# Optimization experiments

Hardware: AMD Instinct MI355X
Metric: run time of the kernel (lower is better)

## Reference

```python
import jax, jax.numpy as jnp
import numpy as np

N_NODES = 100000
N_EDGES = 1600000
IN_FEATS = 128
H_FEATS = 64
N_CONVS = 3
POLY_ORDER = 4
NUM_CLASSES = 2


def setup_inputs() -> dict:
    key = jax.random.key(0)
    ks = jax.random.split(key, 12)
    def w(k, shape):
        fan_in = shape[0]
        return jax.random.normal(k, shape, dtype=jnp.float32) / jnp.sqrt(jnp.float32(fan_in))
    return {
        "feature": jax.random.normal(ks[0], (N_NODES, IN_FEATS), dtype=jnp.float32),
        "src": jax.random.randint(ks[1], (N_EDGES,), 0, N_NODES, dtype=jnp.int32),
        "dst": jax.random.randint(ks[2], (N_EDGES,), 0, N_NODES, dtype=jnp.int32),
        "W1": w(ks[3], (IN_FEATS, H_FEATS)),
        "b1": jnp.zeros((H_FEATS,), dtype=jnp.float32),
        "W2": w(ks[4], (H_FEATS, H_FEATS)),
        "b2": jnp.zeros((H_FEATS,), dtype=jnp.float32),
        "thetas": jax.random.normal(ks[5], (N_CONVS, POLY_ORDER), dtype=jnp.float32) * 0.5,
        "Wm1": w(ks[6], (N_CONVS * H_FEATS, H_FEATS)),
        "bm1": jnp.zeros((H_FEATS,), dtype=jnp.float32),
        "Wm2": w(ks[7], (H_FEATS, NUM_CLASSES)),
        "bm2": jnp.zeros((NUM_CLASSES,), dtype=jnp.float32),
    }


def _poly_conv(theta, feat, src, dst, d_invsqrt, n_nodes):
    # h = sum_k theta[k] * L^k feat, L = I - D^-1/2 A D^-1/2 (applied iteratively)
    out = theta[0] * feat
    for k in range(1, theta.shape[0]):
        m = feat * d_invsqrt                      # [N, H]
        agg = jax.ops.segment_sum(m[src], dst, num_segments=n_nodes)  # copy_u -> sum
        feat = feat - agg * d_invsqrt
        out = out + theta[k] * feat
    return out


def reference(feature, src, dst, W1, b1, W2, b2, thetas, Wm1, bm1, Wm2, bm2):
    n_nodes = feature.shape[0]
    # in-degrees, clamp(min=1), D^-1/2
    deg = jax.ops.segment_sum(jnp.ones_like(dst, dtype=jnp.float32), dst, num_segments=n_nodes)
    d_invsqrt = jnp.power(jnp.clip(deg, 1.0, None), -0.5)[:, None]   # [N, 1]
    # ChiGNN trunk: linear -> ReLU -> linear2 -> ReLU
    h = jax.nn.relu(feature @ W1 + b1)
    h = jax.nn.relu(h @ W2 + b2)
    # N_CONVS polynomial convolutions, concatenated on feature axis
    h_final = jnp.concatenate(
        [_poly_conv(thetas[i], h, src, dst, d_invsqrt, n_nodes) for i in range(thetas.shape[0])],
        axis=-1,
    )  # [N, N_CONVS * H]
    # 2-layer MLP head
    out = jax.nn.relu(h_final @ Wm1 + bm1) @ Wm2 + bm2   # [N, num_classes]
    return out
```

## Files before the change

kernel.cpp:

```cpp
#include <hip/hip_runtime.h>
#include <hip/hip_fp16.h>
#include <math.h>

#define N_NODES 100000
#define N_EDGES 1600000
#define IN_FEATS 128
#define H_FEATS 64
#define NBUK 500
#define BSZ 200
#define NBA 512
#define ACHUNK 3125

typedef _Float16 f16x8 __attribute__((ext_vector_type(8)));
typedef float f32x4 __attribute__((ext_vector_type(4)));

__global__ __launch_bounds__(256) void bucketA_kernel(const int* __restrict__ dst,
                                                      int* __restrict__ blkcnt) {
    __shared__ int cnt[NBUK];
    int t = threadIdx.x;
    for (int i = t; i < NBUK; i += 256) cnt[i] = 0;
    __syncthreads();
    int e0 = blockIdx.x * ACHUNK;
    for (int e = e0 + t; e < e0 + ACHUNK; e += 256)
        atomicAdd(&cnt[dst[e] / BSZ], 1);
    __syncthreads();
    for (int i = t; i < NBUK; i += 256)
        blkcnt[blockIdx.x * NBUK + i] = cnt[i];
}

__global__ __launch_bounds__(512) void bucketB1_kernel(const int* __restrict__ blkcnt,
                                                       int* __restrict__ boff,
                                                       int* __restrict__ buktot) {
    __shared__ int tmp[512];
    int b = blockIdx.x;
    int t = threadIdx.x;
    int v = blkcnt[t * NBUK + b];
    tmp[t] = v;
    __syncthreads();
    #pragma unroll
    for (int off = 1; off < 512; off <<= 1) {
        int x = (t >= off) ? tmp[t - off] : 0;
        __syncthreads();
        tmp[t] += x;
        __syncthreads();
    }
    boff[t * NBUK + b] = tmp[t] - v;
    if (t == 511) buktot[b] = tmp[511];
}

__global__ __launch_bounds__(512) void bucketB2_kernel(const int* __restrict__ buktot,
                                                       int* __restrict__ bukbase,
                                                       int* __restrict__ rowp) {
    __shared__ int tmp[512];
    int t = threadIdx.x;
    int v = (t < NBUK) ? buktot[t] : 0;
    tmp[t] = v;
    __syncthreads();
    #pragma unroll
    for (int off = 1; off < 512; off <<= 1) {
        int x = (t >= off) ? tmp[t - off] : 0;
        __syncthreads();
        tmp[t] += x;
        __syncthreads();
    }
    if (t < NBUK) bukbase[t] = tmp[t] - v;
    if (t == 0) rowp[N_NODES] = N_EDGES;
}

__global__ __launch_bounds__(256) void bucketC_kernel(const int* __restrict__ src,
                                                      const int* __restrict__ dst,
                                                      const int* __restrict__ boff,
                                                      const int* __restrict__ bukbase,
                                                      int* __restrict__ ebuck) {
    __shared__ int sbase[NBUK];
    __shared__ int cur[NBUK];
    int t = threadIdx.x;
    for (int i = t; i < NBUK; i += 256) {
        sbase[i] = bukbase[i] + boff[blockIdx.x * NBUK + i];
        cur[i] = 0;
    }
    __syncthreads();
    int e0 = blockIdx.x * ACHUNK;
    for (int e = e0 + t; e < e0 + ACHUNK; e += 256) {
        int d = dst[e];
        int b = d / BSZ;
        int r = atomicAdd(&cur[b], 1);
        ebuck[sbase[b] + r] = (src[e] << 8) | (d - b * BSZ);
    }
}

__global__ __launch_bounds__(256) void bucketD1_kernel(const int* __restrict__ ebuck,
                                                       const int* __restrict__ bukbase,
                                                       const int* __restrict__ buktot,
                                                       int* __restrict__ rowp,
                                                       float* __restrict__ dinv) {
    __shared__ int deg[BSZ];
    __shared__ int tmp[256];
    int t = threadIdx.x;
    int buk = blockIdx.x;
    int nlo = buk * BSZ;
    int base = bukbase[buk];
    int cnt = buktot[buk];
    for (int i = t; i < BSZ; i += 256) deg[i] = 0;
    __syncthreads();
    for (int k = t; k < cnt; k += 256)
        atomicAdd(&deg[ebuck[base + k] & 255], 1);
    __syncthreads();
    int v = (t < BSZ) ? deg[t] : 0;
    tmp[t] = v;
    __syncthreads();
    #pragma unroll
    for (int off = 1; off < 256; off <<= 1) {
        int x = (t >= off) ? tmp[t - off] : 0;
        __syncthreads();
        tmp[t] += x;
        __syncthreads();
    }
    if (t < BSZ) {
        rowp[nlo + t] = base + tmp[t] - v;
        dinv[nlo + t] = rsqrtf(fmaxf((float)v, 1.0f));
    }
}

__global__ __launch_bounds__(256) void bucketD2_kernel(const int* __restrict__ ebuck,
                                                       const int* __restrict__ bukbase,
                                                       const int* __restrict__ buktot,
                                                       const int* __restrict__ rowp,
                                                       const float* __restrict__ dinv,
                                                       int2* __restrict__ epack) {
    __shared__ int rp[BSZ];
    __shared__ int cur2[BSZ];
    int t = threadIdx.x;
    int buk = blockIdx.x;
    int nlo = buk * BSZ;
    int base = bukbase[buk];
    int cnt = buktot[buk];
    for (int i = t; i < BSZ; i += 256) { rp[i] = rowp[nlo + i]; cur2[i] = 0; }
    __syncthreads();
    for (int k = t; k < cnt; k += 256) {
        int p = ebuck[base + k];
        int ld = p & 255;
        int s = p >> 8;
        int r = atomicAdd(&cur2[ld], 1);
        epack[rp[ld] + r] = make_int2(s, __float_as_int(dinv[s]));
    }
}

__global__ __launch_bounds__(256) void prep_kernel(const float* __restrict__ thetas,
                                                   const float* __restrict__ Wm1,
                                                   const float* __restrict__ W1,
                                                   const float* __restrict__ W2,
                                                   __half* __restrict__ Bpack,
                                                   __half* __restrict__ W1p,
                                                   __half* __restrict__ W2p) {
    int u = blockIdx.x * 256 + threadIdx.x;
    if (u < 16384) {
        int j = u & 7, lane = (u >> 3) & 63, frag = u >> 9;
        int nt = frag & 3, s = frag >> 2;
        int k = 32 * s + ((lane >> 4) << 3) + j;
        int q = k >> 6, f = k & 63;
        int n = nt * 16 + (lane & 15);
        float acc = 0.f;
        #pragma unroll
        for (int c = 0; c < 3; ++c)
            acc = fmaf(thetas[c * 4 + q], Wm1[(c * 64 + f) * 64 + n], acc);
        Bpack[u] = __float2half(acc);
    } else if (u < 16384 + 8192) {
        int v = u - 16384;
        int j = v & 7, lane = (v >> 3) & 63, frag = v >> 9;
        int nt = frag & 3, s = frag >> 2;
        int k = 32 * s + ((lane >> 4) << 3) + j;
        int n = nt * 16 + (lane & 15);
        W1p[v] = __float2half(W1[k * 64 + n]);
    } else if (u < 16384 + 8192 + 4096) {
        int v = u - 24576;
        int j = v & 7, lane = (v >> 3) & 63, frag = v >> 9;
        int nt = frag & 3, s2 = frag >> 2;
        int k = 32 * s2 + ((lane >> 4) << 3) + j;
        int n = nt * 16 + (lane & 15);
        W2p[v] = __float2half(W2[k * 64 + n]);
    }
}

__global__ __launch_bounds__(256) void trunk_mfma_kernel(
    const float* __restrict__ X, const __half* __restrict__ W1p, const float* __restrict__ b1,
    const __half* __restrict__ W2p, const float* __restrict__ b2, __half* __restrict__ H)
{
    __shared__ __half hl[4][1024];
    int t = threadIdx.x;
    int wv = t >> 6, lane = t & 63;
    int r_lo = lane & 15;
    int g = lane >> 4;
    char* myl = (char*)hl[wv];

    int tile = blockIdx.x * 4 + wv;
    if (tile >= 6250) return;

    const f16x8* w1f = (const f16x8*)W1p;
    const f16x8* w2f = (const f16x8*)W2p;
    f16x8 w1b[16], w2b[8];
    #pragma unroll
    for (int f = 0; f < 16; ++f) w1b[f] = w1f[f * 64 + lane];
    #pragma unroll
    for (int f = 0; f < 8; ++f)  w2b[f] = w2f[f * 64 + lane];
    float b1v[4], b2v[4];
    #pragma unroll
    for (int nt = 0; nt < 4; ++nt) {
        b1v[nt] = b1[nt * 16 + r_lo];
        b2v[nt] = b2[nt * 16 + r_lo];
    }

    int row0 = tile * 16;
    const float* xb = X + (size_t)(row0 + r_lo) * IN_FEATS + g * 8;
    f16x8 a1[4];
    #pragma unroll
    for (int s = 0; s < 4; ++s) {
        float4 f0 = *(const float4*)(xb + 32 * s);
        float4 f1 = *(const float4*)(xb + 32 * s + 4);
        f16x8 a;
        a[0] = (_Float16)f0.x; a[1] = (_Float16)f0.y;
        a[2] = (_Float16)f0.z; a[3] = (_Float16)f0.w;
        a[4] = (_Float16)f1.x; a[5] = (_Float16)f1.y;
        a[6] = (_Float16)f1.z; a[7] = (_Float16)f1.w;
        a1[s] = a;
    }
    f32x4 acc1[4];
    #pragma unroll
    for (int nt = 0; nt < 4; ++nt) acc1[nt] = (f32x4){0.f, 0.f, 0.f, 0.f};
    #pragma unroll
    for (int s = 0; s < 4; ++s)
        #pragma unroll
        for (int nt = 0; nt < 4; ++nt)
            acc1[nt] = __builtin_amdgcn_mfma_f32_16x16x32_f16(a1[s], w1b[s * 4 + nt], acc1[nt], 0, 0, 0);
    #pragma unroll
    for (int nt = 0; nt < 4; ++nt)
        #pragma unroll
        for (int reg = 0; reg < 4; ++reg) {
            int r = g * 4 + reg;
            int c = nt * 16 + r_lo;
            int byte = (r * 128 + c * 2) ^ ((r & 7) << 4);
            *(__half*)(myl + byte) = __float2half(fmaxf(acc1[nt][reg] + b1v[nt], 0.f));
        }
    f16x8 a2[2];
    #pragma unroll
    for (int s2 = 0; s2 < 2; ++s2) {
        int byte = (r_lo * 128 + 64 * s2 + g * 16) ^ ((r_lo & 7) << 4);
        a2[s2] = *(const f16x8*)(myl + byte);
    }
    f32x4 acc2[4];
    #pragma unroll
    for (int nt = 0; nt < 4; ++nt) acc2[nt] = (f32x4){0.f, 0.f, 0.f, 0.f};
    #pragma unroll
    for (int s2 = 0; s2 < 2; ++s2)
        #pragma unroll
        for (int nt = 0; nt < 4; ++nt)
            acc2[nt] = __builtin_amdgcn_mfma_f32_16x16x32_f16(a2[s2], w2b[s2 * 4 + nt], acc2[nt], 0, 0, 0);
    #pragma unroll
    for (int nt = 0; nt < 4; ++nt)
        #pragma unroll
        for (int reg = 0; reg < 4; ++reg) {
            int r = g * 4 + reg;
            int c = nt * 16 + r_lo;
            int byte = (r * 128 + c * 2) ^ ((r & 7) << 4);
            *(__half*)(myl + byte) = __float2half(fmaxf(acc2[nt][reg] + b2v[nt], 0.f));
        }
    #pragma unroll
    for (int h2 = 0; h2 < 2; ++h2) {
        int R = (lane >> 3) + 8 * h2;
        int w = lane & 7;
        int byte = (R * 128 + 16 * (w ^ (R & 7)));
        f16x8 hv = *(const f16x8*)(myl + byte);
        *(f16x8*)(H + (size_t)(row0 + R) * 64 + w * 8) = hv;
    }
}

__global__ __launch_bounds__(256) void gather_kernel(
    const __half* __restrict__ Fprev, const int* __restrict__ rowp,
    const int2* __restrict__ epack, const float* __restrict__ dinv,
    __half* __restrict__ Fnew)
{
    int wv = __builtin_amdgcn_readfirstlane(threadIdx.x >> 6);
    int wid = blockIdx.x * 4 + wv;
    int lane = threadIdx.x & 63;
    int beg = rowp[wid], end = rowp[wid + 1];
    float acc = 0.0f;
    int j = beg;
    for (; j + 15 < end; j += 16) {
        int2 e[16];
        #pragma unroll
        for (int q = 0; q < 16; ++q) e[q] = epack[j + q];
        float v[16];
        #pragma unroll
        for (int q = 0; q < 16; ++q)
            v[q] = __half2float(Fprev[(size_t)e[q].x * 64 + lane]);
        #pragma unroll
        for (int q = 0; q < 16; ++q)
            acc = fmaf(v[q], __int_as_float(e[q].y), acc);
    }
    for (; j + 7 < end; j += 8) {
        int2 e[8];
        #pragma unroll
        for (int q = 0; q < 8; ++q) e[q] = epack[j + q];
        float v[8];
        #pragma unroll
        for (int q = 0; q < 8; ++q)
            v[q] = __half2float(Fprev[(size_t)e[q].x * 64 + lane]);
        #pragma unroll
        for (int q = 0; q < 8; ++q)
            acc = fmaf(v[q], __int_as_float(e[q].y), acc);
    }
    for (; j + 3 < end; j += 4) {
        int2 e[4];
        #pragma unroll
        for (int q = 0; q < 4; ++q) e[q] = epack[j + q];
        float v[4];
        #pragma unroll
        for (int q = 0; q < 4; ++q)
            v[q] = __half2float(Fprev[(size_t)e[q].x * 64 + lane]);
        #pragma unroll
        for (int q = 0; q < 4; ++q)
            acc = fmaf(v[q], __int_as_float(e[q].y), acc);
    }
    for (; j < end; ++j) {
        int2 e = epack[j];
        acc = fmaf(__half2float(Fprev[(size_t)e.x * 64 + lane]), __int_as_float(e.y), acc);
    }
    float self = __half2float(Fprev[(size_t)wid * 64 + lane]);
    Fnew[(size_t)wid * 64 + lane] = __float2half(self - acc * dinv[wid]);
}

__global__ __launch_bounds__(256) void final_mfma_kernel(
    const __half* __restrict__ L0h, const __half* __restrict__ Bpack,
    const float* __restrict__ Wm2, const float* __restrict__ bm1,
    const float* __restrict__ bm2, float* __restrict__ out)
{
    const size_t NH = (size_t)N_NODES * 64;
    int t = threadIdx.x;
    int wv = t >> 6;
    int lane = t & 63;
    int tile = blockIdx.x * 4 + wv;
    if (tile >= 6250) return;

    const f16x8* bp = (const f16x8*)Bpack;
    f16x8 b[4][8];
    #pragma unroll
    for (int s = 0; s < 8; ++s)
        #pragma unroll
        for (int nt = 0; nt < 4; ++nt)
            b[nt][s] = bp[(s * 4 + nt) * 64 + lane];

    float bm1v[4], w20[4], w21[4];
    #pragma unroll
    for (int nt = 0; nt < 4; ++nt) {
        int n = nt * 16 + (lane & 15);
        bm1v[nt] = bm1[n];
        w20[nt] = Wm2[n * 2 + 0];
        w21[nt] = Wm2[n * 2 + 1];
    }
    float bm20 = bm2[0], bm21 = bm2[1];

    int row0 = tile * 16;
    const __half* abase = L0h + (size_t)(row0 + (lane & 15)) * 64 + ((lane >> 4) << 3);
    f16x8 a[8];
    #pragma unroll
    for (int s = 0; s < 8; ++s)
        a[s] = *(const f16x8*)(abase + (size_t)(s >> 1) * NH + 32 * (s & 1));
    f32x4 acc[4];
    #pragma unroll
    for (int nt = 0; nt < 4; ++nt) acc[nt] = (f32x4){0.f, 0.f, 0.f, 0.f};
    #pragma unroll
    for (int s = 0; s < 8; ++s)
        #pragma unroll
        for (int nt = 0; nt < 4; ++nt)
            acc[nt] = __builtin_amdgcn_mfma_f32_16x16x32_f16(a[s], b[nt][s], acc[nt], 0, 0, 0);
    float o0[4], o1[4];
    #pragma unroll
    for (int reg = 0; reg < 4; ++reg) { o0[reg] = 0.f; o1[reg] = 0.f; }
    #pragma unroll
    for (int nt = 0; nt < 4; ++nt)
        #pragma unroll
        for (int reg = 0; reg < 4; ++reg) {
            float v = fmaxf(acc[nt][reg] + bm1v[nt], 0.f);
            o0[reg] = fmaf(v, w20[nt], o0[reg]);
            o1[reg] = fmaf(v, w21[nt], o1[reg]);
        }
    #pragma unroll
    for (int reg = 0; reg < 4; ++reg) {
        #pragma unroll
        for (int m = 8; m > 0; m >>= 1) {
            o0[reg] += __shfl_xor(o0[reg], m);
            o1[reg] += __shfl_xor(o1[reg], m);
        }
    }
    if ((lane & 15) == 0) {
        int rbase = row0 + (lane >> 4) * 4;
        #pragma unroll
        for (int reg = 0; reg < 4; ++reg) {
            out[(rbase + reg) * 2 + 0] = o0[reg] + bm20;
            out[(rbase + reg) * 2 + 1] = o1[reg] + bm21;
        }
    }
}

extern "C" void kernel_launch(void* const* d_in, const int* in_sizes, int n_in,
                              void* d_out, int out_size, void* d_ws, size_t ws_size,
                              hipStream_t stream)
{
    const float* feature = (const float*)d_in[0];
    const int*   src     = (const int*)d_in[1];
    const int*   dst     = (const int*)d_in[2];
    const float* W1      = (const float*)d_in[3];
    const float* b1      = (const float*)d_in[4];
    const float* W2      = (const float*)d_in[5];
    const float* b2      = (const float*)d_in[6];
    const float* thetas  = (const float*)d_in[7];
    const float* Wm1     = (const float*)d_in[8];
    const float* bm1     = (const float*)d_in[9];
    const float* Wm2     = (const float*)d_in[10];
    const float* bm2     = (const float*)d_in[11];
    float* out = (float*)d_out;

    const size_t NH = (size_t)N_NODES * H_FEATS;
    const int NPAD = 100352;
    float*  dinv    = (float*)d_ws;
    int*    rowp    = (int*)(dinv + NPAD);
    int*    blkcnt  = rowp + NPAD;
    int*    boff    = blkcnt + NBA * NBUK;
    int*    buktot  = boff + NBA * NBUK;
    int*    bukbase = buktot + 512;
    int*    ebuck   = bukbase + 512;
    int2*   epack   = (int2*)(ebuck + N_EDGES);
    __half* Lh      = (__half*)(epack + N_EDGES);
    __half* Bpack   = Lh + 4 * NH;
    __half* W1p     = Bpack + 16384;
    __half* W2p     = W1p + 8192;

    prep_kernel<<<112, 256, 0, stream>>>(thetas, Wm1, W1, W2, Bpack, W1p, W2p);
    trunk_mfma_kernel<<<1563, 256, 0, stream>>>(feature, W1p, b1, W2p, b2, Lh);

    bucketA_kernel<<<NBA, 256, 0, stream>>>(dst, blkcnt);
    bucketB1_kernel<<<NBUK, 512, 0, stream>>>(blkcnt, boff, buktot);
    bucketB2_kernel<<<1, 512, 0, stream>>>(buktot, bukbase, rowp);
    bucketC_kernel<<<NBA, 256, 0, stream>>>(src, dst, boff, bukbase, ebuck);
    bucketD1_kernel<<<NBUK, 256, 0, stream>>>(ebuck, bukbase, buktot, rowp, dinv);
    bucketD2_kernel<<<NBUK, 256, 0, stream>>>(ebuck, bukbase, buktot, rowp, dinv, epack);

    for (int k = 1; k <= 3; ++k)
        gather_kernel<<<25000, 256, 0, stream>>>(Lh + (size_t)(k - 1) * NH, rowp, epack,
                                                 dinv, Lh + (size_t)k * NH);

    final_mfma_kernel<<<1563, 256, 0, stream>>>(Lh, Bpack, Wm2, bm1, bm2, out);
}
```

Measured before the change: 212.0 us.

## Merge CSR fill into degree kernel and drop packed per-edge weights

The two bucket-D kernels are fused into one, so row pointers stay in shared memory and one launch plus a global reload of rowp go away. The CSR edge array now stores only the source index instead of a (src, dinv[src]) pair, which halves the edge stream and removes the dinv gather during construction. In exchange, the gather kernel now does an extra dependent load of dinv[src] per edge, adding a little latency to each unrolled batch. That dinv array is small and likely to stay cached.

Result: slower. 238.2 us (+12.4%).

```diff
diff --git a/kernel.cpp b/kernel.cpp
--- a/kernel.cpp
+++ b/kernel.cpp
@@ -89,19 +89,22 @@
     }
 }
 
-__global__ __launch_bounds__(256) void bucketD1_kernel(const int* __restrict__ ebuck,
-                                                       const int* __restrict__ bukbase,
-                                                       const int* __restrict__ buktot,
-                                                       int* __restrict__ rowp,
-                                                       float* __restrict__ dinv) {
+__global__ __launch_bounds__(256) void bucketD_kernel(const int* __restrict__ ebuck,
+                                                      const int* __restrict__ bukbase,
+                                                      const int* __restrict__ buktot,
+                                                      int* __restrict__ rowp,
+                                                      float* __restrict__ dinv,
+                                                      int* __restrict__ esrc) {
     __shared__ int deg[BSZ];
     __shared__ int tmp[256];
+    __shared__ int rp[BSZ];
+    __shared__ int cur2[BSZ];
     int t = threadIdx.x;
     int buk = blockIdx.x;
     int nlo = buk * BSZ;
     int base = bukbase[buk];
     int cnt = buktot[buk];
-    for (int i = t; i < BSZ; i += 256) deg[i] = 0;
+    for (int i = t; i < BSZ; i += 256) { deg[i] = 0; cur2[i] = 0; }
     __syncthreads();
     for (int k = t; k < cnt; k += 256)
         atomicAdd(&deg[ebuck[base + k] & 255], 1);
@@ -117,32 +120,17 @@
         __syncthreads();
     }
     if (t < BSZ) {
-        rowp[nlo + t] = base + tmp[t] - v;
+        int rbase = base + tmp[t] - v;
+        rp[t] = rbase;
+        rowp[nlo + t] = rbase;
         dinv[nlo + t] = rsqrtf(fmaxf((float)v, 1.0f));
     }
-}
-
-__global__ __launch_bounds__(256) void bucketD2_kernel(const int* __restrict__ ebuck,
-                                                       const int* __restrict__ bukbase,
-                                                       const int* __restrict__ buktot,
-                                                       const int* __restrict__ rowp,
-                                                       const float* __restrict__ dinv,
-                                                       int2* __restrict__ epack) {
-    __shared__ int rp[BSZ];
-    __shared__ int cur2[BSZ];
-    int t = threadIdx.x;
-    int buk = blockIdx.x;
-    int nlo = buk * BSZ;
-    int base = bukbase[buk];
-    int cnt = buktot[buk];
-    for (int i = t; i < BSZ; i += 256) { rp[i] = rowp[nlo + i]; cur2[i] = 0; }
     __syncthreads();
     for (int k = t; k < cnt; k += 256) {
         int p = ebuck[base + k];
         int ld = p & 255;
-        int s = p >> 8;
         int r = atomicAdd(&cur2[ld], 1);
-        epack[rp[ld] + r] = make_int2(s, __float_as_int(dinv[s]));
+        esrc[rp[ld] + r] = p >> 8;
     }
 }
 
@@ -276,7 +264,7 @@
 
 __global__ __launch_bounds__(256) void gather_kernel(
     const __half* __restrict__ Fprev, const int* __restrict__ rowp,
-    const int2* __restrict__ epack, const float* __restrict__ dinv,
+    const int* __restrict__ esrc, const float* __restrict__ dinv,
     __half* __restrict__ Fnew)
 {
     int wv = __builtin_amdgcn_readfirstlane(threadIdx.x >> 6);
@@ -286,44 +274,53 @@
     float acc = 0.0f;
     int j = beg;
     for (; j + 15 < end; j += 16) {
-        int2 e[16];
-        #pragma unroll
-        for (int q = 0; q < 16; ++q) e[q] = epack[j + q];
+        int s[16];
+        #pragma unroll
+        for (int q = 0; q < 16; ++q) s[q] = esrc[j + q];
+        float w[16];
+        #pragma unroll
+        for (int q = 0; q < 16; ++q) w[q] = dinv[s[q]];
         float v[16];
         #pragma unroll
         for (int q = 0; q < 16; ++q)
-            v[q] = __half2float(Fprev[(size_t)e[q].x * 64 + lane]);
+            v[q] = __half2float(Fprev[(size_t)s[q] * 64 + lane]);
         #pragma unroll
         for (int q = 0; q < 16; ++q)
-            acc = fmaf(v[q], __int_as_float(e[q].y), acc);
+            acc = fmaf(v[q], w[q], acc);
     }
     for (; j + 7 < end; j += 8) {
-        int2 e[8];
-        #pragma unroll
-        for (int q = 0; q < 8; ++q) e[q] = epack[j + q];
+        int s[8];
+        #pragma unroll
+        for (int q = 0; q < 8; ++q) s[q] = esrc[j + q];
+        float w[8];
+        #pragma unroll
+        for (int q = 0; q < 8; ++q) w[q] = dinv[s[q]];
         float v[8];
         #pragma unroll
         for (int q = 0; q < 8; ++q)
-            v[q] = __half2float(Fprev[(size_t)e[q].x * 64 + lane]);
+            v[q] = __half2float(Fprev[(size_t)s[q] * 64 + lane]);
         #pragma unroll
         for (int q = 0; q < 8; ++q)
-            acc = fmaf(v[q], __int_as_float(e[q].y), acc);
+            acc = fmaf(v[q], w[q], acc);
     }
     for (; j + 3 < end; j += 4) {
-        int2 e[4];
-        #pragma unroll
-        for (int q = 0; q < 4; ++q) e[q] = epack[j + q];
+        int s[4];
+        #pragma unroll
+        for (int q = 0; q < 4; ++q) s[q] = esrc[j + q];
+        float w[4];
+        #pragma unroll
+        for (int q = 0; q < 4; ++q) w[q] = dinv[s[q]];
         float v[4];
         #pragma unroll
         for (int q = 0; q < 4; ++q)
-            v[q] = __half2float(Fprev[(size_t)e[q].x * 64 + lane]);
+            v[q] = __half2float(Fprev[(size_t)s[q] * 64 + lane]);
         #pragma unroll
         for (int q = 0; q < 4; ++q)
-            acc = fmaf(v[q], __int_as_float(e[q].y), acc);
+            acc = fmaf(v[q], w[q], acc);
     }
     for (; j < end; ++j) {
-        int2 e = epack[j];
-        acc = fmaf(__half2float(Fprev[(size_t)e.x * 64 + lane]), __int_as_float(e.y), acc);
+        int s = esrc[j];
+        acc = fmaf(__half2float(Fprev[(size_t)s * 64 + lane]), dinv[s], acc);
     }
     float self = __half2float(Fprev[(size_t)wid * 64 + lane]);
     Fnew[(size_t)wid * 64 + lane] = __float2half(self - acc * dinv[wid]);
@@ -429,8 +426,8 @@
     int*    buktot  = boff + NBA * NBUK;
     int*    bukbase = buktot + 512;
     int*    ebuck   = bukbase + 512;
-    int2*   epack   = (int2*)(ebuck + N_EDGES);
-    __half* Lh      = (__half*)(epack + N_EDGES);
+    int*    esrc    = ebuck + N_EDGES;
+    __half* Lh      = (__half*)(esrc + N_EDGES);
     __half* Bpack   = Lh + 4 * NH;
     __half* W1p     = Bpack + 16384;
     __half* W2p     = W1p + 8192;
@@ -442,11 +439,10 @@
     bucketB1_kernel<<<NBUK, 512, 0, stream>>>(blkcnt, boff, buktot);
     bucketB2_kernel<<<1, 512, 0, stream>>>(buktot, bukbase, rowp);
     bucketC_kernel<<<NBA, 256, 0, stream>>>(src, dst, boff, bukbase, ebuck);
-    bucketD1_kernel<<<NBUK, 256, 0, stream>>>(ebuck, bukbase, buktot, rowp, dinv);
-    bucketD2_kernel<<<NBUK, 256, 0, stream>>>(ebuck, bukbase, buktot, rowp, dinv, epack);
+    bucketD_kernel<<<NBUK, 256, 0, stream>>>(ebuck, bukbase, buktot, rowp, dinv, esrc);
 
     for (int k = 1; k <= 3; ++k)
-        gather_kernel<<<25000, 256, 0, stream>>>(Lh + (size_t)(k - 1) * NH, rowp, epack,
+        gather_kernel<<<25000, 256, 0, stream>>>(Lh + (size_t)(k - 1) * NH, rowp, esrc,
                                                  dinv, Lh + (size_t)k * NH);
 
     final_mfma_kernel<<<1563, 256, 0, stream>>>(Lh, Bpack, Wm2, bm1, bm2, out);
```
